# Kernel optimization log

Measured on AMD Instinct MI355X. Metric: run time of the kernel, lower is better.

## Reference

```python
import jax, jax.numpy as jnp
import numpy as np

KERNEL_SIZE = 3
DILATIONS = (1, 2, 3)


def setup_inputs() -> dict:
    key = jax.random.key(0)
    k0, k1, k2 = jax.random.split(key, 3)
    B, N, C = 16, 4096, 256
    x = jax.random.normal(k0, (B, N, C), jnp.float32)
    Wqkv = jax.random.normal(k1, (len(DILATIONS), C, 3 * C), jnp.float32) * 0.02
    Wproj = jax.random.normal(k2, (C, C), jnp.float32) * 0.02
    bproj = jnp.zeros((C,), jnp.float32)
    return {"x": x, "Wqkv": Wqkv, "Wproj": Wproj, "bproj": bproj}


def _window(t, dilation, ksize):
    """Gather dilated local windows along the token axis.
    t: (B, N, C) -> (B, N, ksize, C), zero-padded (matches nn.Unfold padding)."""
    B, N, C = t.shape
    pad = dilation * (ksize - 1) // 2
    tp = jnp.pad(t, ((0, 0), (pad, pad), (0, 0)))
    # idx[n, j] = n + j*dilation  indexes into the padded sequence
    idx = jnp.arange(N)[:, None] + jnp.arange(ksize)[None, :] * dilation  # (N, K)
    return tp[:, idx, :]  # (B, N, K, C)


def reference(x, Wqkv, Wproj, bproj):
    B, N, C = x.shape
    scale = C ** (-0.5)
    outs = []
    for i, d in enumerate(DILATIONS):
        qkv = x @ Wqkv[i]                      # (B, N, 3C)
        q, k, v = jnp.split(qkv, 3, axis=-1)   # each (B, N, C)
        kw = _window(k, d, KERNEL_SIZE)        # (B, N, K, C)
        vw = _window(v, d, KERNEL_SIZE)        # (B, N, K, C)
        logits = jnp.einsum('bnc,bnkc->bnk', q, kw) * scale
        attn = jax.nn.softmax(logits, axis=-1)  # (B, N, K)
        outs.append(jnp.einsum('bnk,bnkc->bnc', attn, vw))
    combined = jnp.mean(jnp.stack(outs, axis=0), axis=0)  # mean over dilation branches
    return combined @ Wproj + bproj
```

## Files before the change

kernel.cpp:

```cpp
#include <hip/hip_runtime.h>
#include <hip/hip_bf16.h>
#include <math.h>

#define BB 16
#define NN 4096
#define CC 256
#define NC 768
#define MTOT (BB * NN)

typedef __attribute__((ext_vector_type(8))) __bf16 bf16x8;
typedef __attribute__((ext_vector_type(4))) float f32x4;

__device__ __forceinline__ unsigned short f2bf(float f) {
    union { float f; unsigned int u; } v; v.f = f;
    unsigned int r = (v.u + 0x7FFFu + ((v.u >> 16) & 1u)) >> 16;
    return (unsigned short)r;
}
__device__ __forceinline__ float bf2f(unsigned short b) {
    union { unsigned int u; float f; } v; v.u = ((unsigned int)b) << 16;
    return v.f;
}

#define GL16(gp, lp) \
    __builtin_amdgcn_global_load_lds((const __attribute__((address_space(1))) void*)(gp), \
                                     (__attribute__((address_space(3))) void*)(lp), 16, 0, 0)

template<int KDIM>
__device__ __forceinline__ void gemm_tile(const unsigned short* __restrict__ A,
                                          const unsigned short* __restrict__ Bt,
                                          int bm, int bn,
                                          unsigned short* As, unsigned short* Bs,
                                          f32x4 (&acc)[4][4]) {
    const int tid = threadIdx.x;
    const int lane = tid & 63;
    const int wave = tid >> 6;
    const int q = lane >> 4;
    const int r16 = lane & 15;
    const int wm = (wave >> 1) * 64;
    const int wn = (wave & 1) * 64;

    const int e0 = tid, e1 = tid + 256;
    const int r0 = e0 >> 2, r1 = e1 >> 2;
    const int kc0 = (e0 & 3) ^ ((r0 >> 1) & 3);
    const int kc1 = (e1 & 3) ^ ((r1 >> 1) & 3);
    const unsigned short* gA0 = A + (size_t)(bm + r0) * KDIM + kc0 * 8;
    const unsigned short* gA1 = A + (size_t)(bm + r1) * KDIM + kc1 * 8;
    const unsigned short* gB0 = Bt + (size_t)(bn + r0) * KDIM + kc0 * 8;
    const unsigned short* gB1 = Bt + (size_t)(bn + r1) * KDIM + kc1 * 8;

    const int sw = (q ^ ((r16 >> 1) & 3)) * 8;

    for (int kt = 0; kt < KDIM; kt += 32) {
        if (kt) __syncthreads();
        GL16(gA0 + kt, As + e0 * 8);
        GL16(gA1 + kt, As + e1 * 8);
        GL16(gB0 + kt, Bs + e0 * 8);
        GL16(gB1 + kt, Bs + e1 * 8);
        __syncthreads();

        bf16x8 af[4], bfr[4];
#pragma unroll
        for (int mi = 0; mi < 4; ++mi)
            af[mi] = *(const bf16x8*)(As + (wm + mi * 16 + r16) * 32 + sw);
#pragma unroll
        for (int ni = 0; ni < 4; ++ni)
            bfr[ni] = *(const bf16x8*)(Bs + (wn + ni * 16 + r16) * 32 + sw);
#pragma unroll
        for (int mi = 0; mi < 4; ++mi)
#pragma unroll
            for (int ni = 0; ni < 4; ++ni)
                acc[mi][ni] = __builtin_amdgcn_mfma_f32_16x16x32_bf16(
                    af[mi], bfr[ni], acc[mi][ni], 0, 0, 0);
    }
}

__global__ __launch_bounds__(256) void conv_all(const float* __restrict__ Wqkv,
                                                const float* __restrict__ Wproj,
                                                unsigned short* __restrict__ Wqb,
                                                unsigned short* __restrict__ Wkb,
                                                unsigned short* __restrict__ Wvs,
                                                unsigned short* __restrict__ WpT) {
    int t = blockIdx.x * 256 + threadIdx.x;
    if (t < 3 * CC * NC) {
        unsigned short v = f2bf(Wqkv[t]);
        int ic = t / NC;
        int col = t - ic * NC;
        if (col < 256)       Wqb[(size_t)ic * CC + col] = v;
        else if (col < 512)  Wkb[(size_t)ic * CC + col - 256] = v;
        else                 Wvs[(size_t)ic * CC + col - 512] = v;
    } else {
        int e = t - 3 * CC * NC;
        int g = e >> 8, c = e & 255;
        WpT[e] = f2bf(Wproj[(size_t)c * CC + g]);
    }
}

__global__ __launch_bounds__(256) void wgemm(const unsigned short* __restrict__ Wqb,
                                             const unsigned short* __restrict__ Wkb,
                                             const unsigned short* __restrict__ Wvs,
                                             const unsigned short* __restrict__ WpT,
                                             unsigned short* __restrict__ MtY,
                                             unsigned short* __restrict__ PtZ) {
    const int z = blockIdx.z;
    const unsigned short *A, *Bt;
    unsigned short* C;
    int nout; float mult;
    if (z < 3) {
        if (blockIdx.x >= 2) return;
        A = Wkb + z * CC * CC; Bt = Wqb + z * CC * CC; C = MtY + z * CC * CC;
        nout = CC; mult = 0.0625f;
    } else {
        A = WpT; Bt = Wvs; C = PtZ;
        nout = NC; mult = 1.0f / 3.0f;
    }

    __shared__ unsigned short As[128 * 32];
    __shared__ unsigned short Bs[128 * 32];
    f32x4 acc[4][4];
#pragma unroll
    for (int i = 0; i < 4; ++i)
#pragma unroll
        for (int j = 0; j < 4; ++j) acc[i][j] = {0.f, 0.f, 0.f, 0.f};

    gemm_tile<CC>(A, Bt, blockIdx.y * 128, blockIdx.x * 128, As, Bs, acc);

    const int lane = threadIdx.x & 63;
    const int wave = threadIdx.x >> 6;
    const int q = lane >> 4, r16 = lane & 15;
    const int wm = (wave >> 1) * 64, wn = (wave & 1) * 64;
#pragma unroll
    for (int mi = 0; mi < 4; ++mi)
#pragma unroll
        for (int ni = 0; ni < 4; ++ni) {
            int row0 = blockIdx.y * 128 + wm + mi * 16 + q * 4;
            int col = blockIdx.x * 128 + wn + ni * 16 + r16;
#pragma unroll
            for (int r = 0; r < 4; ++r)
                C[(size_t)(row0 + r) * nout + col] = f2bf(acc[mi][ni][r] * mult);
        }
}

__global__ __launch_bounds__(256, 2) void mega(const float* __restrict__ xf,
                                               const unsigned short* __restrict__ MtY,
                                               const unsigned short* __restrict__ PtZ,
                                               const float* __restrict__ bias,
                                               float* __restrict__ out) {
    __shared__ __align__(16) unsigned short xbuf[70 * 264];
    __shared__ __align__(16) unsigned short bstage[4 * 4096];
    __shared__ __align__(16) unsigned short yseg[4 * 16 * 72];
    __shared__ __align__(16) float wsm[64 * 4];

    const int tid = threadIdx.x;
    const int lane = tid & 63;
    const int wave = tid >> 6;
    const int q = lane >> 4;
    const int r16 = lane & 15;
    const int t0 = blockIdx.x * 64;

    const int colA = tid >> 2;
    const int kcA = (tid & 3) ^ ((colA >> 1) & 3);
    const unsigned short* mBase  = MtY + (size_t)colA * CC + kcA * 8;
    const unsigned short* pBase0 = PtZ + (size_t)colA * NC + kcA * 8;
    const unsigned short* pBase1 = PtZ + (size_t)(colA + 64) * NC + kcA * 8;

    auto issue_stage = [&](int gs) {
        if (gs >= 96) return;
        unsigned short* dst = bstage + (gs & 3) * 4096 + tid * 8;
        const int i2 = gs >> 5;
        const int r = gs & 31;
        if (r < 16) {
            const unsigned short* src =
                mBase + (size_t)(i2 * 256 + (r >> 2) * 64) * CC + (r & 3) * 64;
            GL16(src, dst);
            GL16(src + 32, dst + 2048);
        } else {
            const int r2 = r - 16;
            const size_t off = (size_t)(r2 & 1) * (128 * NC) + i2 * 256 + (r2 >> 1) * 32;
            GL16(pBase0 + off, dst);
            GL16(pBase1 + off, dst + 2048);
        }
    };

    issue_stage(0); issue_stage(1); issue_stage(2);

    for (int it = 0; it < 9; ++it) {
        int e = it * 256 + tid;
        if (e < 2240) {
            int rr = e >> 5, c = e & 31;
            int gr = t0 - 3 + rr;
            gr = gr < 0 ? 0 : (gr > MTOT - 1 ? MTOT - 1 : gr);
            const float* xp = xf + (size_t)gr * CC + c * 8;
            float4 a = *(const float4*)xp;
            float4 b = *(const float4*)(xp + 4);
            unsigned short p[8];
            p[0] = f2bf(a.x); p[1] = f2bf(a.y); p[2] = f2bf(a.z); p[3] = f2bf(a.w);
            p[4] = f2bf(b.x); p[5] = f2bf(b.y); p[6] = f2bf(b.z); p[7] = f2bf(b.w);
            *(float4*)(xbuf + rr * 264 + c * 8) = *(const float4*)p;
        }
    }
    __syncthreads();

    bf16x8 af[8];
#pragma unroll
    for (int kt = 0; kt < 8; ++kt)
        af[kt] = *(const bf16x8*)(xbuf + (3 + wave * 16 + r16) * 264 + kt * 32 + q * 8);

    f32x4 oacc[16];
#pragma unroll
    for (int j = 0; j < 16; ++j) oacc[j] = {0.f, 0.f, 0.f, 0.f};

    const int fragsw = q ^ ((r16 >> 1) & 3);
    int gctr = 3;
    int sctr = 0;

#pragma unroll 1
    for (int i = 0; i < 3; ++i) {
        const int dil = i + 1;
        f32x4 lacc[3];
#pragma unroll
        for (int j = 0; j < 3; ++j) lacc[j] = {0.f, 0.f, 0.f, 0.f};

#pragma unroll
        for (int cq = 0; cq < 4; ++cq) {
            f32x4 yacc[4];
#pragma unroll
            for (int nf = 0; nf < 4; ++nf) yacc[nf] = {0.f, 0.f, 0.f, 0.f};
#pragma unroll
            for (int ktp = 0; ktp < 4; ++ktp) {
                asm volatile("s_waitcnt vmcnt(4)" ::: "memory");
                __builtin_amdgcn_s_barrier();
                __builtin_amdgcn_sched_barrier(0);
                issue_stage(gctr); ++gctr;
                const unsigned short* bp = bstage + (sctr & 3) * 4096;
                ++sctr;
                __builtin_amdgcn_s_setprio(1);
#pragma unroll
                for (int kt2 = 0; kt2 < 2; ++kt2)
#pragma unroll
                    for (int nf = 0; nf < 4; ++nf) {
                        bf16x8 b = *(const bf16x8*)(bp + kt2 * 2048 +
                                        ((nf * 16 + r16) * 4 + fragsw) * 8);
                        yacc[nf] = __builtin_amdgcn_mfma_f32_16x16x32_bf16(
                            af[ktp * 2 + kt2], b, yacc[nf], 0, 0, 0);
                    }
                __builtin_amdgcn_s_setprio(0);
            }
            unsigned short* ys = yseg + wave * (16 * 72);
#pragma unroll
            for (int nf = 0; nf < 4; ++nf)
#pragma unroll
                for (int rr = 0; rr < 4; ++rr)
                    ys[(q * 4 + rr) * 72 + nf * 16 + r16] = f2bf(yacc[nf][rr]);
            asm volatile("s_waitcnt lgkmcnt(0)" ::: "memory");
            __builtin_amdgcn_sched_barrier(0);
            bf16x8 ya0 = *(const bf16x8*)(ys + r16 * 72 + q * 8);
            bf16x8 ya1 = *(const bf16x8*)(ys + r16 * 72 + 32 + q * 8);
#pragma unroll
            for (int j = 0; j < 3; ++j) {
                const unsigned short* xr =
                    xbuf + (3 + wave * 16 + r16 + (j - 1) * dil) * 264 + cq * 64 + q * 8;
                bf16x8 xb0 = *(const bf16x8*)xr;
                bf16x8 xb1 = *(const bf16x8*)(xr + 32);
                lacc[j] = __builtin_amdgcn_mfma_f32_16x16x32_bf16(ya0, xb0, lacc[j], 0, 0, 0);
                lacc[j] = __builtin_amdgcn_mfma_f32_16x16x32_bf16(ya1, xb1, lacc[j], 0, 0, 0);
            }
        }

        {
            const int rr = r16 & 3;
            float l0 = rr == 0 ? lacc[0][0] : rr == 1 ? lacc[0][1] : rr == 2 ? lacc[0][2] : lacc[0][3];
            float l1 = rr == 0 ? lacc[1][0] : rr == 1 ? lacc[1][1] : rr == 2 ? lacc[1][2] : lacc[1][3];
            float l2 = rr == 0 ? lacc[2][0] : rr == 1 ? lacc[2][1] : rr == 2 ? lacc[2][2] : lacc[2][3];
            const int ns = (t0 + wave * 16 + r16) & (NN - 1);
            const bool vlo = ns >= dil;
            const bool vhi = ns + dil < NN;
            l0 = vlo ? l0 : 0.f;
            l2 = vhi ? l2 : 0.f;
            float mx = fmaxf(l0, fmaxf(l1, l2));
            float e0 = __expf(l0 - mx), e1 = __expf(l1 - mx), e2 = __expf(l2 - mx);
            float inv = 1.0f / (e0 + e1 + e2);
            if (q == (r16 >> 2)) {
                float* wq = wsm + (wave * 16 + r16) * 4;
                wq[0] = vlo ? e0 * inv : 0.f;
                wq[1] = e1 * inv;
                wq[2] = vhi ? e2 * inv : 0.f;
            }
        }
        asm volatile("s_waitcnt lgkmcnt(0)" ::: "memory");
        __builtin_amdgcn_sched_barrier(0);
        const float* wp = wsm + (wave * 16 + r16) * 4;
        const float w0 = wp[0], w1 = wp[1], w2 = wp[2];

#pragma unroll
        for (int kt = 0; kt < 8; ++kt) {
            const unsigned short* xr1 =
                xbuf + (3 + wave * 16 + r16) * 264 + kt * 32 + q * 8;
            bf16x8 a0 = *(const bf16x8*)(xr1 - dil * 264);
            bf16x8 a1 = *(const bf16x8*)(xr1);
            bf16x8 a2 = *(const bf16x8*)(xr1 + dil * 264);
            const unsigned short* u0 = (const unsigned short*)&a0;
            const unsigned short* u1 = (const unsigned short*)&a1;
            const unsigned short* u2 = (const unsigned short*)&a2;
            union { unsigned short s[8]; bf16x8 v; } za;
#pragma unroll
            for (int e = 0; e < 8; ++e)
                za.s[e] = f2bf(w0 * bf2f(u0[e]) + w1 * bf2f(u1[e]) + w2 * bf2f(u2[e]));
#pragma unroll
            for (int cqp = 0; cqp < 2; ++cqp) {
                asm volatile("s_waitcnt vmcnt(4)" ::: "memory");
                __builtin_amdgcn_s_barrier();
                __builtin_amdgcn_sched_barrier(0);
                issue_stage(gctr); ++gctr;
                const unsigned short* bp = bstage + (sctr & 3) * 4096;
                ++sctr;
                __builtin_amdgcn_s_setprio(1);
#pragma unroll
                for (int cq2 = 0; cq2 < 2; ++cq2)
#pragma unroll
                    for (int nf = 0; nf < 4; ++nf) {
                        const int col = cq2 * 64 + nf * 16 + r16;
                        bf16x8 b = *(const bf16x8*)(bp + (col * 4 + fragsw) * 8);
                        oacc[(cqp * 2 + cq2) * 4 + nf] =
                            __builtin_amdgcn_mfma_f32_16x16x32_bf16(
                                za.v, b, oacc[(cqp * 2 + cq2) * 4 + nf], 0, 0, 0);
                    }
                __builtin_amdgcn_s_setprio(0);
            }
        }
    }

#pragma unroll
    for (int cq = 0; cq < 4; ++cq)
#pragma unroll
        for (int nf = 0; nf < 4; ++nf) {
            int gc = cq * 64 + nf * 16 + r16;
            float bc = bias[gc];
            f32x4 v = oacc[cq * 4 + nf];
#pragma unroll
            for (int r = 0; r < 4; ++r)
                out[(size_t)(t0 + wave * 16 + q * 4 + r) * CC + gc] = v[r] + bc;
        }
}

extern "C" void kernel_launch(void* const* d_in, const int* in_sizes, int n_in,
                              void* d_out, int out_size, void* d_ws, size_t ws_size,
                              hipStream_t stream) {
    const float* x = (const float*)d_in[0];
    const float* Wqkv = (const float*)d_in[1];
    const float* Wproj = (const float*)d_in[2];
    const float* bproj = (const float*)d_in[3];
    float* out = (float*)d_out;

    unsigned short* Wqb = (unsigned short*)d_ws;
    unsigned short* Wkb = Wqb + (size_t)3 * CC * CC;
    unsigned short* Wvs = Wkb + (size_t)3 * CC * CC;
    unsigned short* WpT = Wvs + (size_t)3 * CC * CC;
    unsigned short* MtY = WpT + (size_t)CC * CC;
    unsigned short* PtZ = MtY + (size_t)NC * CC;

    conv_all<<<(3 * CC * NC + CC * CC) / 256, 256, 0, stream>>>(
        Wqkv, Wproj, Wqb, Wkb, Wvs, WpT);
    wgemm<<<dim3(6, 2, 4), 256, 0, stream>>>(Wqb, Wkb, Wvs, WpT, MtY, PtZ);
    mega<<<MTOT / 64, 256, 0, stream>>>(x, MtY, PtZ, bproj, out);
}
```

Baseline: 214.0 us.

## Repartition waves by output column and overlap logit reduction with QK stages

Each wave now owns a 64-column slice for all 64 tokens instead of 16 tokens across all columns. One B-fragment load is reused across four token fragments, and logits become per-wave partial sums reduced through shared memory. The B staging ring shrinks from four buffers to three, the MtY stage ordering is permuted to match, and logit and softmax work is interleaved with stages. The trade-off is that only one or two waves issue MFMAs per barrier-synchronised stage, so work is serialised across waves and the prefetch depth is shallower.

After: 323.2 us. 1.51x slower.

```diff
diff --git a/kernel.cpp b/kernel.cpp
--- a/kernel.cpp
+++ b/kernel.cpp
@@ -146,13 +146,13 @@
                                                const float* __restrict__ bias,
                                                float* __restrict__ out) {
     __shared__ __align__(16) unsigned short xbuf[70 * 264];
-    __shared__ __align__(16) unsigned short bstage[4 * 4096];
+    __shared__ __align__(16) unsigned short bstage[3 * 4096];
     __shared__ __align__(16) unsigned short yseg[4 * 16 * 72];
-    __shared__ __align__(16) float wsm[64 * 4];
+    __shared__ __align__(16) float part[4][64][3];
 
     const int tid = threadIdx.x;
     const int lane = tid & 63;
-    const int wave = tid >> 6;
+    const int wn = tid >> 6;
     const int q = lane >> 4;
     const int r16 = lane & 15;
     const int t0 = blockIdx.x * 64;
@@ -165,12 +165,12 @@
 
     auto issue_stage = [&](int gs) {
         if (gs >= 96) return;
-        unsigned short* dst = bstage + (gs & 3) * 4096 + tid * 8;
+        unsigned short* dst = bstage + (gs % 3) * 4096 + tid * 8;
         const int i2 = gs >> 5;
         const int r = gs & 31;
         if (r < 16) {
             const unsigned short* src =
-                mBase + (size_t)(i2 * 256 + (r >> 2) * 64) * CC + (r & 3) * 64;
+                mBase + (size_t)(i2 * 256 + (r & 3) * 64) * CC + (r >> 2) * 64;
             GL16(src, dst);
             GL16(src + 32, dst + 2048);
         } else {
@@ -181,7 +181,7 @@
         }
     };
 
-    issue_stage(0); issue_stage(1); issue_stage(2);
+    issue_stage(0); issue_stage(1);
 
     for (int it = 0; it < 9; ++it) {
         int e = it * 256 + tid;
@@ -200,145 +200,176 @@
     }
     __syncthreads();
 
-    bf16x8 af[8];
-#pragma unroll
-    for (int kt = 0; kt < 8; ++kt)
-        af[kt] = *(const bf16x8*)(xbuf + (3 + wave * 16 + r16) * 264 + kt * 32 + q * 8);
-
     f32x4 oacc[16];
 #pragma unroll
     for (int j = 0; j < 16; ++j) oacc[j] = {0.f, 0.f, 0.f, 0.f};
 
     const int fragsw = q ^ ((r16 >> 1) & 3);
-    int gctr = 3;
     int sctr = 0;
 
 #pragma unroll 1
     for (int i = 0; i < 3; ++i) {
         const int dil = i + 1;
-        f32x4 lacc[3];
-#pragma unroll
-        for (int j = 0; j < 3; ++j) lacc[j] = {0.f, 0.f, 0.f, 0.f};
-
-#pragma unroll
-        for (int cq = 0; cq < 4; ++cq) {
-            f32x4 yacc[4];
-#pragma unroll
-            for (int nf = 0; nf < 4; ++nf) yacc[nf] = {0.f, 0.f, 0.f, 0.f};
-#pragma unroll
-            for (int ktp = 0; ktp < 4; ++ktp) {
-                asm volatile("s_waitcnt vmcnt(4)" ::: "memory");
-                __builtin_amdgcn_s_barrier();
+        f32x4 yacc[16];
+#pragma unroll
+        for (int j = 0; j < 16; ++j) yacc[j] = {0.f, 0.f, 0.f, 0.f};
+        float wgt[4][3];
+
+        auto logit_work = [&]() {
+            unsigned short* ys = yseg + wn * (16 * 72);
+#pragma unroll
+            for (int tf = 0; tf < 4; ++tf) {
+#pragma unroll
+                for (int nf = 0; nf < 4; ++nf)
+#pragma unroll
+                    for (int rr = 0; rr < 4; ++rr)
+                        ys[(q * 4 + rr) * 72 + nf * 16 + r16] =
+                            f2bf(yacc[tf * 4 + nf][rr]);
+                asm volatile("s_waitcnt lgkmcnt(0)" ::: "memory");
                 __builtin_amdgcn_sched_barrier(0);
-                issue_stage(gctr); ++gctr;
-                const unsigned short* bp = bstage + (sctr & 3) * 4096;
-                ++sctr;
+                bf16x8 ya0 = *(const bf16x8*)(ys + r16 * 72 + q * 8);
+                bf16x8 ya1 = *(const bf16x8*)(ys + r16 * 72 + 32 + q * 8);
+                f32x4 lacc[3];
+#pragma unroll
+                for (int j = 0; j < 3; ++j) lacc[j] = {0.f, 0.f, 0.f, 0.f};
+#pragma unroll
+                for (int j = 0; j < 3; ++j) {
+                    const unsigned short* xr =
+                        xbuf + (3 + tf * 16 + r16 + (j - 1) * dil) * 264 + wn * 64 + q * 8;
+                    lacc[j] = __builtin_amdgcn_mfma_f32_16x16x32_bf16(
+                        ya0, *(const bf16x8*)xr, lacc[j], 0, 0, 0);
+                    lacc[j] = __builtin_amdgcn_mfma_f32_16x16x32_bf16(
+                        ya1, *(const bf16x8*)(xr + 32), lacc[j], 0, 0, 0);
+                }
+                if (q == (r16 >> 2)) {
+                    const int rr = r16 & 3;
+                    float p0 = rr == 0 ? lacc[0][0] : rr == 1 ? lacc[0][1] : rr == 2 ? lacc[0][2] : lacc[0][3];
+                    float p1 = rr == 0 ? lacc[1][0] : rr == 1 ? lacc[1][1] : rr == 2 ? lacc[1][2] : lacc[1][3];
+                    float p2 = rr == 0 ? lacc[2][0] : rr == 1 ? lacc[2][1] : rr == 2 ? lacc[2][2] : lacc[2][3];
+                    part[wn][tf * 16 + r16][0] = p0;
+                    part[wn][tf * 16 + r16][1] = p1;
+                    part[wn][tf * 16 + r16][2] = p2;
+                }
+            }
+            asm volatile("s_waitcnt lgkmcnt(0)" ::: "memory");
+        };
+
+        for (int sl = 0; sl < 16; ++sl) {
+            asm volatile("s_waitcnt vmcnt(2)" ::: "memory");
+            __builtin_amdgcn_s_barrier();
+            __builtin_amdgcn_sched_barrier(0);
+            issue_stage(sctr + 2);
+            const int ktp = sl >> 2, cq = sl & 3;
+            if (cq == wn) {
+                const unsigned short* bp = bstage + (sctr % 3) * 4096;
+#pragma unroll
+                for (int kk = 0; kk < 2; ++kk) {
+                    bf16x8 bfr[4], afv[4];
+#pragma unroll
+                    for (int nf = 0; nf < 4; ++nf)
+                        bfr[nf] = *(const bf16x8*)(bp + kk * 2048 +
+                                      ((nf * 16 + r16) * 4 + fragsw) * 8);
+#pragma unroll
+                    for (int tf = 0; tf < 4; ++tf)
+                        afv[tf] = *(const bf16x8*)(xbuf + (3 + tf * 16 + r16) * 264 +
+                                      ktp * 64 + kk * 32 + q * 8);
+                    __builtin_amdgcn_s_setprio(1);
+#pragma unroll
+                    for (int tf = 0; tf < 4; ++tf)
+#pragma unroll
+                        for (int nf = 0; nf < 4; ++nf)
+                            yacc[tf * 4 + nf] = __builtin_amdgcn_mfma_f32_16x16x32_bf16(
+                                afv[tf], bfr[nf], yacc[tf * 4 + nf], 0, 0, 0);
+                    __builtin_amdgcn_s_setprio(0);
+                }
+            }
+            if (ktp == 3 && wn < 3 && cq == wn + 1) logit_work();
+            ++sctr;
+        }
+
+        __builtin_amdgcn_s_barrier();
+        __builtin_amdgcn_sched_barrier(0);
+        if (wn == 3) logit_work();
+
+        for (int sl = 0; sl < 16; ++sl) {
+            asm volatile("s_waitcnt vmcnt(2)" ::: "memory");
+            __builtin_amdgcn_s_barrier();
+            __builtin_amdgcn_sched_barrier(0);
+            issue_stage(sctr + 2);
+            const int kt = sl >> 1, cqp = sl & 1;
+            if (sl == 0) {
+#pragma unroll
+                for (int tf = 0; tf < 4; ++tf) {
+                    const int tok = tf * 16 + r16;
+                    float l0 = part[0][tok][0] + part[1][tok][0] +
+                               part[2][tok][0] + part[3][tok][0];
+                    float l1 = part[0][tok][1] + part[1][tok][1] +
+                               part[2][tok][1] + part[3][tok][1];
+                    float l2 = part[0][tok][2] + part[1][tok][2] +
+                               part[2][tok][2] + part[3][tok][2];
+                    const int ns = (t0 + tok) & (NN - 1);
+                    const bool vlo = ns >= dil;
+                    const bool vhi = ns + dil < NN;
+                    l0 = vlo ? l0 : 0.f;
+                    l2 = vhi ? l2 : 0.f;
+                    float mx = fmaxf(l0, fmaxf(l1, l2));
+                    float e0 = __expf(l0 - mx), e1 = __expf(l1 - mx), e2 = __expf(l2 - mx);
+                    float inv = 1.0f / (e0 + e1 + e2);
+                    wgt[tf][0] = vlo ? e0 * inv : 0.f;
+                    wgt[tf][1] = e1 * inv;
+                    wgt[tf][2] = vhi ? e2 * inv : 0.f;
+                }
+            }
+            if (cqp == (wn >> 1)) {
+                const unsigned short* bp = bstage + (sctr % 3) * 4096;
+                union { unsigned int w[4]; bf16x8 v; } za[4];
+#pragma unroll
+                for (int tf = 0; tf < 4; ++tf) {
+                    const unsigned short* xr1 =
+                        xbuf + (3 + tf * 16 + r16) * 264 + kt * 32 + q * 8;
+                    bf16x8 a0 = *(const bf16x8*)(xr1 - dil * 264);
+                    bf16x8 a1 = *(const bf16x8*)(xr1);
+                    bf16x8 a2 = *(const bf16x8*)(xr1 + dil * 264);
+                    const unsigned short* u0 = (const unsigned short*)&a0;
+                    const unsigned short* u1 = (const unsigned short*)&a1;
+                    const unsigned short* u2 = (const unsigned short*)&a2;
+                    const float w0 = wgt[tf][0], w1 = wgt[tf][1], w2 = wgt[tf][2];
+#pragma unroll
+                    for (int e2i = 0; e2i < 4; ++e2i) {
+                        float zl = w0 * bf2f(u0[e2i * 2]) + w1 * bf2f(u1[e2i * 2]) +
+                                   w2 * bf2f(u2[e2i * 2]);
+                        float zh = w0 * bf2f(u0[e2i * 2 + 1]) + w1 * bf2f(u1[e2i * 2 + 1]) +
+                                   w2 * bf2f(u2[e2i * 2 + 1]);
+                        asm("v_cvt_pk_bf16_f32 %0, %1, %2"
+                            : "=v"(za[tf].w[e2i]) : "v"(zl), "v"(zh));
+                    }
+                }
                 __builtin_amdgcn_s_setprio(1);
 #pragma unroll
-                for (int kt2 = 0; kt2 < 2; ++kt2)
-#pragma unroll
-                    for (int nf = 0; nf < 4; ++nf) {
-                        bf16x8 b = *(const bf16x8*)(bp + kt2 * 2048 +
-                                        ((nf * 16 + r16) * 4 + fragsw) * 8);
-                        yacc[nf] = __builtin_amdgcn_mfma_f32_16x16x32_bf16(
-                            af[ktp * 2 + kt2], b, yacc[nf], 0, 0, 0);
-                    }
+                for (int nf = 0; nf < 4; ++nf) {
+                    bf16x8 b = *(const bf16x8*)(bp + (wn & 1) * 2048 +
+                                    ((nf * 16 + r16) * 4 + fragsw) * 8);
+#pragma unroll
+                    for (int tf = 0; tf < 4; ++tf)
+                        oacc[tf * 4 + nf] = __builtin_amdgcn_mfma_f32_16x16x32_bf16(
+                            za[tf].v, b, oacc[tf * 4 + nf], 0, 0, 0);
+                }
                 __builtin_amdgcn_s_setprio(0);
             }
-            unsigned short* ys = yseg + wave * (16 * 72);
-#pragma unroll
-            for (int nf = 0; nf < 4; ++nf)
-#pragma unroll
-                for (int rr = 0; rr < 4; ++rr)
-                    ys[(q * 4 + rr) * 72 + nf * 16 + r16] = f2bf(yacc[nf][rr]);
-            asm volatile("s_waitcnt lgkmcnt(0)" ::: "memory");
-            __builtin_amdgcn_sched_barrier(0);
-            bf16x8 ya0 = *(const bf16x8*)(ys + r16 * 72 + q * 8);
-            bf16x8 ya1 = *(const bf16x8*)(ys + r16 * 72 + 32 + q * 8);
-#pragma unroll
-            for (int j = 0; j < 3; ++j) {
-                const unsigned short* xr =
-                    xbuf + (3 + wave * 16 + r16 + (j - 1) * dil) * 264 + cq * 64 + q * 8;
-                bf16x8 xb0 = *(const bf16x8*)xr;
-                bf16x8 xb1 = *(const bf16x8*)(xr + 32);
-                lacc[j] = __builtin_amdgcn_mfma_f32_16x16x32_bf16(ya0, xb0, lacc[j], 0, 0, 0);
-                lacc[j] = __builtin_amdgcn_mfma_f32_16x16x32_bf16(ya1, xb1, lacc[j], 0, 0, 0);
-            }
-        }
-
-        {
-            const int rr = r16 & 3;
-            float l0 = rr == 0 ? lacc[0][0] : rr == 1 ? lacc[0][1] : rr == 2 ? lacc[0][2] : lacc[0][3];
-            float l1 = rr == 0 ? lacc[1][0] : rr == 1 ? lacc[1][1] : rr == 2 ? lacc[1][2] : lacc[1][3];
-            float l2 = rr == 0 ? lacc[2][0] : rr == 1 ? lacc[2][1] : rr == 2 ? lacc[2][2] : lacc[2][3];
-            const int ns = (t0 + wave * 16 + r16) & (NN - 1);
-            const bool vlo = ns >= dil;
-            const bool vhi = ns + dil < NN;
-            l0 = vlo ? l0 : 0.f;
-            l2 = vhi ? l2 : 0.f;
-            float mx = fmaxf(l0, fmaxf(l1, l2));
-            float e0 = __expf(l0 - mx), e1 = __expf(l1 - mx), e2 = __expf(l2 - mx);
-            float inv = 1.0f / (e0 + e1 + e2);
-            if (q == (r16 >> 2)) {
-                float* wq = wsm + (wave * 16 + r16) * 4;
-                wq[0] = vlo ? e0 * inv : 0.f;
-                wq[1] = e1 * inv;
-                wq[2] = vhi ? e2 * inv : 0.f;
-            }
-        }
-        asm volatile("s_waitcnt lgkmcnt(0)" ::: "memory");
-        __builtin_amdgcn_sched_barrier(0);
-        const float* wp = wsm + (wave * 16 + r16) * 4;
-        const float w0 = wp[0], w1 = wp[1], w2 = wp[2];
-
-#pragma unroll
-        for (int kt = 0; kt < 8; ++kt) {
-            const unsigned short* xr1 =
-                xbuf + (3 + wave * 16 + r16) * 264 + kt * 32 + q * 8;
-            bf16x8 a0 = *(const bf16x8*)(xr1 - dil * 264);
-            bf16x8 a1 = *(const bf16x8*)(xr1);
-            bf16x8 a2 = *(const bf16x8*)(xr1 + dil * 264);
-            const unsigned short* u0 = (const unsigned short*)&a0;
-            const unsigned short* u1 = (const unsigned short*)&a1;
-            const unsigned short* u2 = (const unsigned short*)&a2;
-            union { unsigned short s[8]; bf16x8 v; } za;
-#pragma unroll
-            for (int e = 0; e < 8; ++e)
-                za.s[e] = f2bf(w0 * bf2f(u0[e]) + w1 * bf2f(u1[e]) + w2 * bf2f(u2[e]));
-#pragma unroll
-            for (int cqp = 0; cqp < 2; ++cqp) {
-                asm volatile("s_waitcnt vmcnt(4)" ::: "memory");
-                __builtin_amdgcn_s_barrier();
-                __builtin_amdgcn_sched_barrier(0);
-                issue_stage(gctr); ++gctr;
-                const unsigned short* bp = bstage + (sctr & 3) * 4096;
-                ++sctr;
-                __builtin_amdgcn_s_setprio(1);
-#pragma unroll
-                for (int cq2 = 0; cq2 < 2; ++cq2)
-#pragma unroll
-                    for (int nf = 0; nf < 4; ++nf) {
-                        const int col = cq2 * 64 + nf * 16 + r16;
-                        bf16x8 b = *(const bf16x8*)(bp + (col * 4 + fragsw) * 8);
-                        oacc[(cqp * 2 + cq2) * 4 + nf] =
-                            __builtin_amdgcn_mfma_f32_16x16x32_bf16(
-                                za.v, b, oacc[(cqp * 2 + cq2) * 4 + nf], 0, 0, 0);
-                    }
-                __builtin_amdgcn_s_setprio(0);
-            }
-        }
-    }
-
-#pragma unroll
-    for (int cq = 0; cq < 4; ++cq)
+            ++sctr;
+        }
+    }
+
+#pragma unroll
+    for (int tf = 0; tf < 4; ++tf)
 #pragma unroll
         for (int nf = 0; nf < 4; ++nf) {
-            int gc = cq * 64 + nf * 16 + r16;
+            const int gc = wn * 64 + nf * 16 + r16;
             float bc = bias[gc];
-            f32x4 v = oacc[cq * 4 + nf];
+            f32x4 v = oacc[tf * 4 + nf];
 #pragma unroll
             for (int r = 0; r < 4; ++r)
-                out[(size_t)(t0 + wave * 16 + q * 4 + r) * CC + gc] = v[r] + bc;
+                out[(size_t)(t0 + tf * 16 + q * 4 + r) * CC + gc] = v[r] + bc;
         }
 }
 
```
